# Kernel tuning notes

Hardware: AMD Instinct MI355X
Metric: run time of the kernel (lower is better)

Reference implementation:

```python
import jax, jax.numpy as jnp
import numpy as np

B, T, C = 4, 2048, 1024
N_HEAD = 16
HEAD_DIM = C // N_HEAD

def setup_inputs() -> dict:
    key = jax.random.key(0)
    k1, k2, k3, k4, k5 = jax.random.split(key, 5)
    sigma = (1.0 / C) ** 0.5  # encoder_var=1 default
    return {
        "x": jax.random.normal(k1, (B, T, C), dtype=jnp.float32),
        "W_attn": jax.random.normal(k2, (3 * C, C), dtype=jnp.float32) * sigma,
        "b_attn": jax.random.normal(k3, (3 * C,), dtype=jnp.float32),
        "W_proj": jax.random.normal(k4, (C, C), dtype=jnp.float32) * sigma,
        "b_proj": jax.random.normal(k5, (C,), dtype=jnp.float32),
    }

def reference(x, W_attn, b_attn, W_proj, b_proj):
    Bq, Tq, Cq = x.shape
    qkv = x @ W_attn.T + b_attn              # [B,T,3C]
    q, k, v = jnp.split(qkv, 3, axis=-1)
    def to_heads(t):
        return t.reshape(Bq, Tq, N_HEAD, HEAD_DIM).transpose(0, 2, 1, 3)  # [B,H,T,D]
    q, k, v = to_heads(q), to_heads(k), to_heads(v)
    # NOTE: original scales by 1/head_dim (not 1/sqrt(head_dim))
    att = jnp.einsum('bhqd,bhkd->bhqk', q, k) * (1.0 / HEAD_DIM)
    causal = jnp.tril(jnp.ones((Tq, Tq), dtype=bool))
    att = jnp.where(causal[None, None], att, -jnp.inf)
    att = jax.nn.softmax(att, axis=-1)
    y = jnp.einsum('bhqk,bhkd->bhqd', att, v)
    y = y.transpose(0, 2, 1, 3).reshape(Bq, Tq, Cq)
    return y @ W_proj.T + b_proj
```

## Files before the change

### kernel.cpp

```cpp
#include <hip/hip_runtime.h>

typedef __attribute__((ext_vector_type(8))) short s16x8;
typedef __attribute__((ext_vector_type(4))) float f32x4;
typedef __attribute__((ext_vector_type(4))) unsigned short u16x4;

#define T_  2048
#define C_  1024
#define D_  64

__device__ __forceinline__ unsigned short f2bf(float f){
  union { float fv; unsigned int u; } v; v.fv = f;
  unsigned int r = v.u + 0x7FFFu + ((v.u >> 16) & 1u);
  return (unsigned short)(r >> 16);
}

__device__ __forceinline__ float exp2_asm(float x){
  float r; asm("v_exp_f32 %0, %1" : "=v"(r) : "v"(x)); return r;
}
__device__ __forceinline__ unsigned int cvtpk(float lo, float hi){
  unsigned int r; asm("v_cvt_pk_bf16_f32 %0, %1, %2" : "=v"(r) : "v"(lo), "v"(hi)); return r;
}

__device__ __forceinline__ void gload_lds16(const void* g, void* l){
  __builtin_amdgcn_global_load_lds(
      (const __attribute__((address_space(1))) unsigned int*)g,
      (__attribute__((address_space(3))) unsigned int*)l, 16, 0, 0);
}

__global__ __launch_bounds__(256) void cvt_kernel(const float* __restrict__ src,
                                                  unsigned short* __restrict__ dst){
  size_t i = ((size_t)blockIdx.x * 256u + threadIdx.x) * 8u;
  f32x4 a = *(const f32x4*)(src + i);
  f32x4 b = *(const f32x4*)(src + i + 4);
  s16x8 o;
  #pragma unroll
  for (int j = 0; j < 4; ++j){ o[j] = (short)f2bf(a[j]); o[4+j] = (short)f2bf(b[j]); }
  *(s16x8*)(dst + i) = o;
}

template<int MODE>
__global__ __launch_bounds__(512, 2) void gemm_bt(
    const unsigned short* __restrict__ A, const unsigned short* __restrict__ Bw,
    const float* __restrict__ bias, int M, int N, int K, int nbx,
    unsigned short* __restrict__ q_ws, unsigned short* __restrict__ k_ws,
    unsigned short* __restrict__ vT_ws, float* __restrict__ out)
{
  __shared__ unsigned short Asl[4][256*32];
  __shared__ unsigned short Bsl[4][128*32];
  const int tid = threadIdx.x;
  const int lane = tid & 63, wid = tid >> 6;
  const int g = lane >> 4, lr = lane & 15;
  const int wm = wid >> 1, wn = wid & 1;
  const int nwg = (int)gridDim.x;
  const int cpx = nwg >> 3;
  const int orig = (int)blockIdx.x;
  const int wgid = (orig & 7) * cpx + (orig >> 3);
  const int bx = wgid % nbx, by = wgid / nbx;
  const int m0 = by * 256, n0 = bx * 128;

  f32x4 acc[4][4];
  #pragma unroll
  for (int i = 0; i < 4; ++i)
    #pragma unroll
    for (int j = 0; j < 4; ++j) acc[i][j] = (f32x4){0.f,0.f,0.f,0.f};

  auto stageA = [&](int ks){
    const int slot = ks & 3;
    const size_t kbyte = ((size_t)ks) << 6;
    #pragma unroll
    for (int j = 0; j < 2; ++j){
      const int c = j*512 + tid;
      const int row = c >> 2;
      const int srcq = ((c & 3) - (row >> 1)) & 3;
      gload_lds16((const char*)A + ((size_t)(m0+row)*K)*2 + kbyte + srcq*16,
                  (char*)&Asl[slot][0] + (size_t)c*16);
    }
  };
  auto stageB = [&](int ks){
    const int slot = ks & 3;
    const size_t kbyte = ((size_t)ks) << 6;
    const int c = tid;
    const int row = c >> 2;
    const int srcq = ((c & 3) - (row >> 1)) & 3;
    gload_lds16((const char*)Bw + ((size_t)(n0+row)*K)*2 + kbyte + srcq*16,
                (char*)&Bsl[slot][0] + (size_t)c*16);
  };

  const int nks = K >> 5;
  stageA(0); stageB(0);
  stageA(1); stageB(1);
  stageA(2); stageB(2);
  asm volatile("s_waitcnt vmcnt(6)" ::: "memory");
  asm volatile("s_barrier" ::: "memory");

  for (int ks = 0; ks < nks; ++ks){
    const int slot = ks & 3;
    const char* As = (const char*)&Asl[slot][0];
    const char* Bs = (const char*)&Bsl[slot][0];

    s16x8 af[4], bf[4];
    #pragma unroll
    for (int mi = 0; mi < 4; ++mi){
      const int row = wm*64 + mi*16 + lr;
      af[mi] = *(const s16x8*)(As + row*64 + (((g + (row >> 1)) & 3) << 4));
    }
    #pragma unroll
    for (int ni = 0; ni < 4; ++ni){
      const int row = wn*64 + ni*16 + lr;
      bf[ni] = *(const s16x8*)(Bs + row*64 + (((g + (row >> 1)) & 3) << 4));
    }

    if (ks + 3 < nks){ stageA(ks + 3); stageB(ks + 3); }

    asm volatile("s_waitcnt lgkmcnt(0)" ::: "memory");
    __builtin_amdgcn_s_setprio(1);
    #pragma unroll
    for (int mi = 0; mi < 4; ++mi)
      #pragma unroll
      for (int ni = 0; ni < 4; ++ni)
        acc[mi][ni] = __builtin_amdgcn_mfma_f32_16x16x32_bf16(af[mi], bf[ni], acc[mi][ni], 0, 0, 0);
    __builtin_amdgcn_s_setprio(0);

    if (ks + 1 < nks){
      if (ks + 3 < nks)      asm volatile("s_waitcnt vmcnt(6)" ::: "memory");
      else if (ks + 2 < nks) asm volatile("s_waitcnt vmcnt(3)" ::: "memory");
      else                   asm volatile("s_waitcnt vmcnt(0)" ::: "memory");
      asm volatile("s_barrier" ::: "memory");
    }
  }

  #pragma unroll
  for (int mi = 0; mi < 4; ++mi){
    #pragma unroll
    for (int ni = 0; ni < 4; ++ni){
      const int n = n0 + wn*64 + ni*16 + lr;
      const float bv = bias[n];
      #pragma unroll
      for (int r = 0; r < 4; ++r){
        const int m = m0 + wm*64 + mi*16 + g*4 + r;
        const float val = acc[mi][ni][r] + bv;
        if (MODE == 0){
          const int which = n >> 10;
          const int cc = n & 1023;
          const int h = cc >> 6, d = cc & 63;
          const int bq = m >> 11, t = m & 2047;
          const int bh = bq*16 + h;
          if (which == 0)      q_ws[((size_t)bh*T_ + t)*D_ + d] = f2bf(val * 0.022542110013890054f);
          else if (which == 1) k_ws[((size_t)bh*T_ + t)*D_ + d] = f2bf(val);
          else                 vT_ws[((size_t)bh*D_ + d)*T_ + t] = f2bf(val);
        } else {
          out[(size_t)m*N + n] = val;
        }
      }
    }
  }
}

__global__ __launch_bounds__(256, 4) void attn_kernel(
    const unsigned short* __restrict__ q_ws, const unsigned short* __restrict__ k_ws,
    const unsigned short* __restrict__ vT_ws, unsigned short* __restrict__ y_ws)
{
  __shared__ __align__(16) unsigned short Ks[2][64*64];
  __shared__ __align__(16) unsigned short Vs[2][64*64];

  const int tid = threadIdx.x;
  const int lane = tid & 63, wid = tid >> 6;
  const int g = lane >> 4, lr = lane & 15;
  const int orig = (int)blockIdx.x;
  const int wgid = (orig & 7) * 128 + (orig >> 3);
  const int p  = wgid & 15;
  const int bh = wgid >> 4;
  const int qwA = p*64 + wid*16,  qwB = (31 - p)*64 + wid*16;
  const int qrowA = qwA + lr,     qrowB = qwB + lr;
  const int swz = (lr & 7) << 4;

  const unsigned short* Qb = q_ws  + (size_t)bh*T_*D_;
  const unsigned short* Kb = k_ws  + (size_t)bh*T_*D_;
  const unsigned short* Vb = vT_ws + (size_t)bh*D_*T_;

  auto stage = [&](int t, int buf){
    const int kt0 = t << 6;
    #pragma unroll
    for (int s = 0; s < 2; ++s){
      const int c = s*256 + tid;
      const int r = c >> 3;
      const int scol = ((c & 7) << 4) ^ ((r & 7) << 4);
      gload_lds16((const char*)Kb + ((size_t)(kt0 + r)*D_)*2 + scol,
                  (char*)&Ks[buf][0] + c*16);
      gload_lds16((const char*)Vb + ((size_t)r*T_ + kt0)*2 + scol,
                  (char*)&Vs[buf][0] + c*16);
    }
  };

  const s16x8 bqA0 = *(const s16x8*)&Qb[(size_t)(qwA+lr)*D_ + g*8];
  const s16x8 bqA1 = *(const s16x8*)&Qb[(size_t)(qwA+lr)*D_ + 32 + g*8];
  const s16x8 bqB0 = *(const s16x8*)&Qb[(size_t)(qwB+lr)*D_ + g*8];
  const s16x8 bqB1 = *(const s16x8*)&Qb[(size_t)(qwB+lr)*D_ + 32 + g*8];

  s16x8 ones;
  #pragma unroll
  for (int j = 0; j < 8; ++j) ones[j] = (short)0x3F80;

  f32x4 yA[4], yB[4];
  #pragma unroll
  for (int dt = 0; dt < 4; ++dt){ yA[dt] = (f32x4){0.f,0.f,0.f,0.f}; yB[dt] = (f32x4){0.f,0.f,0.f,0.f}; }
  f32x4 lacA = (f32x4){0.f,0.f,0.f,0.f}, lacB = (f32x4){0.f,0.f,0.f,0.f};
  float mA = -1e30f, mB = -1e30f;

  const int ntA = p + 1, ntB = 32 - p;
  stage(0, 0);
  __syncthreads();

  for (int t = 0; t < ntB; ++t){
    const int cur = t & 1;
    if (t + 1 < ntB) stage(t + 1, cur ^ 1);
    const int kt0 = t << 6;
    const unsigned short* Kt = &Ks[cur][0];
    const unsigned short* Vt = &Vs[cur][0];
    unsigned short* Pw = &Ks[cur][wid*1024];
    const bool actA = (t < ntA);

    f32x4 sB[4], sA[4];
    #pragma unroll
    for (int kk = 0; kk < 4; ++kk){
      const int row = kk*16 + lr;
      const s16x8 a0 = *(const s16x8*)&Kt[row*64 + (((g*16)      ^ swz) >> 1)];
      const s16x8 a1 = *(const s16x8*)&Kt[row*64 + (((64 + g*16) ^ swz) >> 1)];
      f32x4 acc = (f32x4){0.f,0.f,0.f,0.f};
      acc = __builtin_amdgcn_mfma_f32_16x16x32_bf16(a0, bqB0, acc, 0, 0, 0);
      acc = __builtin_amdgcn_mfma_f32_16x16x32_bf16(a1, bqB1, acc, 0, 0, 0);
      sB[kk] = acc;
      if (actA){
        f32x4 acc2 = (f32x4){0.f,0.f,0.f,0.f};
        acc2 = __builtin_amdgcn_mfma_f32_16x16x32_bf16(a0, bqA0, acc2, 0, 0, 0);
        acc2 = __builtin_amdgcn_mfma_f32_16x16x32_bf16(a1, bqA1, acc2, 0, 0, 0);
        sA[kk] = acc2;
      }
    }

    if (kt0 + 63 > qwB){
      #pragma unroll
      for (int kk = 0; kk < 4; ++kk)
        #pragma unroll
        for (int r = 0; r < 4; ++r)
          if (kt0 + kk*16 + g*4 + r > qrowB) sB[kk][r] = -1e30f;
    }
    {
      float m01 = fmaxf(fmaxf(sB[0][0], sB[0][1]), fmaxf(sB[0][2], sB[0][3]));
      float m23 = fmaxf(fmaxf(sB[1][0], sB[1][1]), fmaxf(sB[1][2], sB[1][3]));
      float m45 = fmaxf(fmaxf(sB[2][0], sB[2][1]), fmaxf(sB[2][2], sB[2][3]));
      float m67 = fmaxf(fmaxf(sB[3][0], sB[3][1]), fmaxf(sB[3][2], sB[3][3]));
      float mx = fmaxf(fmaxf(m01, m23), fmaxf(m45, m67));
      mx = fmaxf(mx, __shfl_xor(mx, 16, 64));
      mx = fmaxf(mx, __shfl_xor(mx, 32, 64));
      if (!__all(mx <= mB + 8.f)){
        const float mnew = fmaxf(mB, mx);
        const float corr = exp2_asm(mB - mnew);
        mB = mnew;
        lacB[0] *= corr;
        #pragma unroll
        for (int dt = 0; dt < 4; ++dt)
          #pragma unroll
          for (int r = 0; r < 4; ++r) yB[dt][r] *= corr;
      }
    }
    union { unsigned int u[2]; u16x4 v; } pkB[4];
    #pragma unroll
    for (int kk = 0; kk < 4; ++kk){
      const float e0 = exp2_asm(sB[kk][0] - mB);
      const float e1 = exp2_asm(sB[kk][1] - mB);
      const float e2 = exp2_asm(sB[kk][2] - mB);
      const float e3 = exp2_asm(sB[kk][3] - mB);
      pkB[kk].u[0] = cvtpk(e0, e1);
      pkB[kk].u[1] = cvtpk(e2, e3);
    }

    asm volatile("s_barrier" ::: "memory");

    #pragma unroll
    for (int kk = 0; kk < 4; ++kk)
      *(u16x4*)&Pw[lr*64 + (((kk*32 + g*8) ^ swz) >> 1)] = pkB[kk].v;
    asm volatile("" ::: "memory");
    {
      const s16x8 p0 = *(const s16x8*)&Pw[lr*64 + (((g*16)      ^ swz) >> 1)];
      const s16x8 p1 = *(const s16x8*)&Pw[lr*64 + (((64 + g*16) ^ swz) >> 1)];
      lacB = __builtin_amdgcn_mfma_f32_16x16x32_bf16(ones, p0, lacB, 0, 0, 0);
      lacB = __builtin_amdgcn_mfma_f32_16x16x32_bf16(ones, p1, lacB, 0, 0, 0);
      #pragma unroll
      for (int dt = 0; dt < 4; ++dt){
        const int vrow = dt*16 + lr;
        const s16x8 v0 = *(const s16x8*)&Vt[vrow*64 + (((g*16)      ^ swz) >> 1)];
        const s16x8 v1 = *(const s16x8*)&Vt[vrow*64 + (((64 + g*16) ^ swz) >> 1)];
        yB[dt] = __builtin_amdgcn_mfma_f32_16x16x32_bf16(v0, p0, yB[dt], 0, 0, 0);
        yB[dt] = __builtin_amdgcn_mfma_f32_16x16x32_bf16(v1, p1, yB[dt], 0, 0, 0);
      }
    }

    if (actA){
      if (kt0 + 63 > qwA){
        #pragma unroll
        for (int kk = 0; kk < 4; ++kk)
          #pragma unroll
          for (int r = 0; r < 4; ++r)
            if (kt0 + kk*16 + g*4 + r > qrowA) sA[kk][r] = -1e30f;
      }
      float m01 = fmaxf(fmaxf(sA[0][0], sA[0][1]), fmaxf(sA[0][2], sA[0][3]));
      float m23 = fmaxf(fmaxf(sA[1][0], sA[1][1]), fmaxf(sA[1][2], sA[1][3]));
      float m45 = fmaxf(fmaxf(sA[2][0], sA[2][1]), fmaxf(sA[2][2], sA[2][3]));
      float m67 = fmaxf(fmaxf(sA[3][0], sA[3][1]), fmaxf(sA[3][2], sA[3][3]));
      float mx = fmaxf(fmaxf(m01, m23), fmaxf(m45, m67));
      mx = fmaxf(mx, __shfl_xor(mx, 16, 64));
      mx = fmaxf(mx, __shfl_xor(mx, 32, 64));
      if (!__all(mx <= mA + 8.f)){
        const float mnew = fmaxf(mA, mx);
        const float corr = exp2_asm(mA - mnew);
        mA = mnew;
        lacA[0] *= corr;
        #pragma unroll
        for (int dt = 0; dt < 4; ++dt)
          #pragma unroll
          for (int r = 0; r < 4; ++r) yA[dt][r] *= corr;
      }
      union { unsigned int u[2]; u16x4 v; } pkA[4];
      #pragma unroll
      for (int kk = 0; kk < 4; ++kk){
        const float e0 = exp2_asm(sA[kk][0] - mA);
        const float e1 = exp2_asm(sA[kk][1] - mA);
        const float e2 = exp2_asm(sA[kk][2] - mA);
        const float e3 = exp2_asm(sA[kk][3] - mA);
        pkA[kk].u[0] = cvtpk(e0, e1);
        pkA[kk].u[1] = cvtpk(e2, e3);
      }
      asm volatile("" ::: "memory");
      #pragma unroll
      for (int kk = 0; kk < 4; ++kk)
        *(u16x4*)&Pw[lr*64 + (((kk*32 + g*8) ^ swz) >> 1)] = pkA[kk].v;
      asm volatile("" ::: "memory");
      const s16x8 p0 = *(const s16x8*)&Pw[lr*64 + (((g*16)      ^ swz) >> 1)];
      const s16x8 p1 = *(const s16x8*)&Pw[lr*64 + (((64 + g*16) ^ swz) >> 1)];
      lacA = __builtin_amdgcn_mfma_f32_16x16x32_bf16(ones, p0, lacA, 0, 0, 0);
      lacA = __builtin_amdgcn_mfma_f32_16x16x32_bf16(ones, p1, lacA, 0, 0, 0);
      #pragma unroll
      for (int dt = 0; dt < 4; ++dt){
        const int vrow = dt*16 + lr;
        const s16x8 v0 = *(const s16x8*)&Vt[vrow*64 + (((g*16)      ^ swz) >> 1)];
        const s16x8 v1 = *(const s16x8*)&Vt[vrow*64 + (((64 + g*16) ^ swz) >> 1)];
        yA[dt] = __builtin_amdgcn_mfma_f32_16x16x32_bf16(v0, p0, yA[dt], 0, 0, 0);
        yA[dt] = __builtin_amdgcn_mfma_f32_16x16x32_bf16(v1, p1, yA[dt], 0, 0, 0);
      }
    }

    __syncthreads();
  }

  const int bq = bh >> 4, h = bh & 15;
  {
    const float inv = 1.f / lacB[0];
    #pragma unroll
    for (int dt = 0; dt < 4; ++dt){
      union { unsigned int u[2]; u16x4 v; } w;
      w.u[0] = cvtpk(yB[dt][0]*inv, yB[dt][1]*inv);
      w.u[1] = cvtpk(yB[dt][2]*inv, yB[dt][3]*inv);
      *(u16x4*)&y_ws[((size_t)(bq*T_ + qwB + lr))*C_ + h*64 + dt*16 + g*4] = w.v;
    }
  }
  {
    const float inv = 1.f / lacA[0];
    #pragma unroll
    for (int dt = 0; dt < 4; ++dt){
      union { unsigned int u[2]; u16x4 v; } w;
      w.u[0] = cvtpk(yA[dt][0]*inv, yA[dt][1]*inv);
      w.u[1] = cvtpk(yA[dt][2]*inv, yA[dt][3]*inv);
      *(u16x4*)&y_ws[((size_t)(bq*T_ + qwA + lr))*C_ + h*64 + dt*16 + g*4] = w.v;
    }
  }
}

extern "C" void kernel_launch(void* const* d_in, const int* in_sizes, int n_in,
                              void* d_out, int out_size, void* d_ws, size_t ws_size,
                              hipStream_t stream) {
  const float* x  = (const float*)d_in[0];
  const float* Wa = (const float*)d_in[1];
  const float* ba = (const float*)d_in[2];
  const float* Wp = (const float*)d_in[3];
  const float* bp = (const float*)d_in[4];
  float* out = (float*)d_out;

  char* ws = (char*)d_ws;
  const size_t MB = 1024u*1024u;
  unsigned short* xb  = (unsigned short*)(ws + 0);
  unsigned short* wab = (unsigned short*)(ws + 16*MB);
  unsigned short* wpb = (unsigned short*)(ws + 22*MB);
  unsigned short* qws = (unsigned short*)(ws + 24*MB);
  unsigned short* kws = (unsigned short*)(ws + 40*MB);
  unsigned short* vT  = (unsigned short*)(ws + 56*MB);
  unsigned short* yws = (unsigned short*)(ws + 72*MB);

  cvt_kernel<<<4096, 256, 0, stream>>>(x,  xb);
  cvt_kernel<<<1536, 256, 0, stream>>>(Wa, wab);
  cvt_kernel<<< 512, 256, 0, stream>>>(Wp, wpb);

  gemm_bt<0><<<dim3(768), 512, 0, stream>>>(xb, wab, ba, 8192, 3072, 1024, 24,
                                            qws, kws, vT, nullptr);
  attn_kernel<<<dim3(1024), 256, 0, stream>>>(qws, kws, vT, yws);
  gemm_bt<1><<<dim3(256), 512, 0, stream>>>(yws, wpb, bp, 8192, 1024, 1024, 8,
                                            nullptr, nullptr, nullptr, out);
}
```

Baseline: 198.4 us.

## Enlarge GEMM tiles to 256x256 with ping-pong staged K-half pipeline

The bf16 GEMM moves from a 256x128 tile with a 4-slot, 32-wide K ring to a 256x256 tile. Each warp now computes 128x64 and keeps 8x4 accumulators. Loads for the next 64-wide K step are staged in two double-buffered halves and interleaved with four MFMA phases separated by barriers. The goal is more operand reuse per LDS byte and fewer global reloads of A, but the launch shrinks to 384 and 128 workgroups. That may underfill the 256 CUs on the output projection, and the extra accumulators and 128 KB of LDS raise register and occupancy pressure.

```diff
diff --git a/kernel.cpp b/kernel.cpp
--- a/kernel.cpp
+++ b/kernel.cpp
@@ -26,6 +26,11 @@
       (const __attribute__((address_space(1))) unsigned int*)g,
       (__attribute__((address_space(3))) unsigned int*)l, 16, 0, 0);
 }
+
+#define BARRIER()  asm volatile("s_barrier" ::: "memory")
+#define LGKM0()    do{ asm volatile("s_waitcnt lgkmcnt(0)" ::: "memory"); \
+                       __builtin_amdgcn_sched_barrier(0); }while(0)
+#define VMCNT(n)   asm volatile("s_waitcnt vmcnt(" #n ")" ::: "memory")
 
 __global__ __launch_bounds__(256) void cvt_kernel(const float* __restrict__ src,
                                                   unsigned short* __restrict__ dst){
@@ -45,74 +50,72 @@
     unsigned short* __restrict__ q_ws, unsigned short* __restrict__ k_ws,
     unsigned short* __restrict__ vT_ws, float* __restrict__ out)
 {
-  __shared__ unsigned short Asl[4][256*32];
-  __shared__ unsigned short Bsl[4][128*32];
+  __shared__ unsigned short Ash[2][2][256*32];
+  __shared__ unsigned short Bsh[2][2][256*32];
   const int tid = threadIdx.x;
   const int lane = tid & 63, wid = tid >> 6;
   const int g = lane >> 4, lr = lane & 15;
-  const int wm = wid >> 1, wn = wid & 1;
+  const int wm = wid >> 2, wn = wid & 3;
   const int nwg = (int)gridDim.x;
   const int cpx = nwg >> 3;
   const int orig = (int)blockIdx.x;
   const int wgid = (orig & 7) * cpx + (orig >> 3);
   const int bx = wgid % nbx, by = wgid / nbx;
-  const int m0 = by * 256, n0 = bx * 128;
-
-  f32x4 acc[4][4];
+  const int m0 = by * 256, n0 = bx * 256;
+
+  f32x4 acc[8][4];
   #pragma unroll
-  for (int i = 0; i < 4; ++i)
+  for (int i = 0; i < 8; ++i)
     #pragma unroll
     for (int j = 0; j < 4; ++j) acc[i][j] = (f32x4){0.f,0.f,0.f,0.f};
 
-  auto stageA = [&](int ks){
-    const int slot = ks & 3;
-    const size_t kbyte = ((size_t)ks) << 6;
+  auto stageA = [&](int tt, int ks){
+    unsigned short* base = &Ash[tt & 1][ks][0];
     #pragma unroll
     for (int j = 0; j < 2; ++j){
       const int c = j*512 + tid;
       const int row = c >> 2;
-      const int srcq = ((c & 3) - (row >> 1)) & 3;
-      gload_lds16((const char*)A + ((size_t)(m0+row)*K)*2 + kbyte + srcq*16,
-                  (char*)&Asl[slot][0] + (size_t)c*16);
+      const int q = ((c & 3) - (row >> 1)) & 3;
+      gload_lds16((const char*)A + ((size_t)(m0+row)*K)*2 + (size_t)tt*128 + ks*64 + q*16,
+                  (char*)base + (size_t)c*16);
     }
   };
-  auto stageB = [&](int ks){
-    const int slot = ks & 3;
-    const size_t kbyte = ((size_t)ks) << 6;
-    const int c = tid;
-    const int row = c >> 2;
-    const int srcq = ((c & 3) - (row >> 1)) & 3;
-    gload_lds16((const char*)Bw + ((size_t)(n0+row)*K)*2 + kbyte + srcq*16,
-                (char*)&Bsl[slot][0] + (size_t)c*16);
+  auto stageB = [&](int tt, int ks){
+    unsigned short* base = &Bsh[tt & 1][ks][0];
+    #pragma unroll
+    for (int j = 0; j < 2; ++j){
+      const int c = j*512 + tid;
+      const int row = c >> 2;
+      const int q = ((c & 3) - (row >> 1)) & 3;
+      gload_lds16((const char*)Bw + ((size_t)(n0+row)*K)*2 + (size_t)tt*128 + ks*64 + q*16,
+                  (char*)base + (size_t)c*16);
+    }
   };
-
-  const int nks = K >> 5;
-  stageA(0); stageB(0);
-  stageA(1); stageB(1);
-  stageA(2); stageB(2);
-  asm volatile("s_waitcnt vmcnt(6)" ::: "memory");
-  asm volatile("s_barrier" ::: "memory");
-
-  for (int ks = 0; ks < nks; ++ks){
-    const int slot = ks & 3;
-    const char* As = (const char*)&Asl[slot][0];
-    const char* Bs = (const char*)&Bsl[slot][0];
-
-    s16x8 af[4], bf[4];
-    #pragma unroll
-    for (int mi = 0; mi < 4; ++mi){
-      const int row = wm*64 + mi*16 + lr;
-      af[mi] = *(const s16x8*)(As + row*64 + (((g + (row >> 1)) & 3) << 4));
-    }
-    #pragma unroll
-    for (int ni = 0; ni < 4; ++ni){
-      const int row = wn*64 + ni*16 + lr;
-      bf[ni] = *(const s16x8*)(Bs + row*64 + (((g + (row >> 1)) & 3) << 4));
-    }
-
-    if (ks + 3 < nks){ stageA(ks + 3); stageB(ks + 3); }
-
-    asm volatile("s_waitcnt lgkmcnt(0)" ::: "memory");
+  auto rdA = [&](int buf, int ks, int mi){
+    const int row = wm*128 + mi*16 + lr;
+    return *(const s16x8*)((const char*)&Ash[buf][ks][0] + row*64 + (((g + (row >> 1)) & 3) << 4));
+  };
+  auto rdB = [&](int buf, int ks, int ni){
+    const int row = wn*64 + ni*16 + lr;
+    return *(const s16x8*)((const char*)&Bsh[buf][ks][0] + row*64 + (((g + (row >> 1)) & 3) << 4));
+  };
+
+  const int nk = K >> 6;
+  stageA(0, 0); stageB(0, 0); stageA(0, 1); stageB(0, 1);
+  VMCNT(4);
+  BARRIER();
+
+  s16x8 af[4], bf[4];
+  for (int t = 0; t < nk; ++t){
+    const int buf = t & 1;
+    const bool pre = (t + 1 < nk);
+
+    #pragma unroll
+    for (int mi = 0; mi < 4; ++mi) af[mi] = rdA(buf, 0, mi);
+    #pragma unroll
+    for (int ni = 0; ni < 4; ++ni) bf[ni] = rdB(buf, 0, ni);
+    if (pre) stageA(t + 1, 0);
+    BARRIER(); LGKM0();
     __builtin_amdgcn_s_setprio(1);
     #pragma unroll
     for (int mi = 0; mi < 4; ++mi)
@@ -120,24 +123,61 @@
       for (int ni = 0; ni < 4; ++ni)
         acc[mi][ni] = __builtin_amdgcn_mfma_f32_16x16x32_bf16(af[mi], bf[ni], acc[mi][ni], 0, 0, 0);
     __builtin_amdgcn_s_setprio(0);
-
-    if (ks + 1 < nks){
-      if (ks + 3 < nks)      asm volatile("s_waitcnt vmcnt(6)" ::: "memory");
-      else if (ks + 2 < nks) asm volatile("s_waitcnt vmcnt(3)" ::: "memory");
-      else                   asm volatile("s_waitcnt vmcnt(0)" ::: "memory");
-      asm volatile("s_barrier" ::: "memory");
-    }
+    BARRIER();
+
+    #pragma unroll
+    for (int mi = 0; mi < 4; ++mi) af[mi] = rdA(buf, 0, mi + 4);
+    if (pre) stageB(t + 1, 0);
+    BARRIER(); LGKM0();
+    __builtin_amdgcn_s_setprio(1);
+    #pragma unroll
+    for (int mi = 0; mi < 4; ++mi)
+      #pragma unroll
+      for (int ni = 0; ni < 4; ++ni)
+        acc[mi+4][ni] = __builtin_amdgcn_mfma_f32_16x16x32_bf16(af[mi], bf[ni], acc[mi+4][ni], 0, 0, 0);
+    __builtin_amdgcn_s_setprio(0);
+    if (pre) { VMCNT(4); } else { VMCNT(0); }
+    BARRIER();
+
+    #pragma unroll
+    for (int mi = 0; mi < 4; ++mi) af[mi] = rdA(buf, 1, mi);
+    #pragma unroll
+    for (int ni = 0; ni < 4; ++ni) bf[ni] = rdB(buf, 1, ni);
+    if (pre) stageA(t + 1, 1);
+    BARRIER(); LGKM0();
+    __builtin_amdgcn_s_setprio(1);
+    #pragma unroll
+    for (int mi = 0; mi < 4; ++mi)
+      #pragma unroll
+      for (int ni = 0; ni < 4; ++ni)
+        acc[mi][ni] = __builtin_amdgcn_mfma_f32_16x16x32_bf16(af[mi], bf[ni], acc[mi][ni], 0, 0, 0);
+    __builtin_amdgcn_s_setprio(0);
+    BARRIER();
+
+    #pragma unroll
+    for (int mi = 0; mi < 4; ++mi) af[mi] = rdA(buf, 1, mi + 4);
+    if (pre) stageB(t + 1, 1);
+    BARRIER(); LGKM0();
+    __builtin_amdgcn_s_setprio(1);
+    #pragma unroll
+    for (int mi = 0; mi < 4; ++mi)
+      #pragma unroll
+      for (int ni = 0; ni < 4; ++ni)
+        acc[mi+4][ni] = __builtin_amdgcn_mfma_f32_16x16x32_bf16(af[mi], bf[ni], acc[mi+4][ni], 0, 0, 0);
+    __builtin_amdgcn_s_setprio(0);
+    if (pre) { VMCNT(4); }
+    BARRIER();
   }
 
   #pragma unroll
-  for (int mi = 0; mi < 4; ++mi){
+  for (int mi = 0; mi < 8; ++mi){
     #pragma unroll
     for (int ni = 0; ni < 4; ++ni){
       const int n = n0 + wn*64 + ni*16 + lr;
       const float bv = bias[n];
       #pragma unroll
       for (int r = 0; r < 4; ++r){
-        const int m = m0 + wm*64 + mi*16 + g*4 + r;
+        const int m = m0 + wm*128 + mi*16 + g*4 + r;
         const float val = acc[mi][ni][r] + bv;
         if (MODE == 0){
           const int which = n >> 10;
@@ -400,9 +440,9 @@
   cvt_kernel<<<1536, 256, 0, stream>>>(Wa, wab);
   cvt_kernel<<< 512, 256, 0, stream>>>(Wp, wpb);
 
-  gemm_bt<0><<<dim3(768), 512, 0, stream>>>(xb, wab, ba, 8192, 3072, 1024, 24,
+  gemm_bt<0><<<dim3(384), 512, 0, stream>>>(xb, wab, ba, 8192, 3072, 1024, 12,
                                             qws, kws, vT, nullptr);
   attn_kernel<<<dim3(1024), 256, 0, stream>>>(qws, kws, vT, yws);
-  gemm_bt<1><<<dim3(256), 512, 0, stream>>>(yws, wpb, bp, 8192, 1024, 1024, 8,
+  gemm_bt<1><<<dim3(128), 512, 0, stream>>>(yws, wpb, bp, 8192, 1024, 1024, 4,
                                             nullptr, nullptr, nullptr, out);
 }
```

Result: slower. 216.4 us (+9.1%).
